# Performance work log

Hardware: AMD Instinct MI355X
Metric: run time of the kernel (lower is better)

## Reference

```python
import jax, jax.numpy as jnp
import numpy as np

EPS = 1e-12  # torch F.normalize eps


def setup_inputs() -> dict:
    key = jax.random.key(0)
    k1, k2 = jax.random.split(key)
    b, c, n, h, w = 4, 64, 25, 64, 64
    dims = 64
    x = jax.random.normal(k1, (b, c, n, h, w), dtype=jnp.float32)
    # 1x1 conv weight: Conv2d(channels, dims*3, 1, bias=False) -> [3*dims, channels]
    W = jax.random.normal(k2, (3 * dims, c), dtype=jnp.float32) * 0.05
    return {"x": x, "W": W}


def reference(x, W):
    b, c, n, h, w = x.shape
    N = n * h * w
    # 1x1 conv over channel dim (applied per (b, n) slice == plain channel matmul)
    qkv = jnp.einsum('oc,bcnhw->bonhw', W, x)  # [b, 3d, n, h, w]
    q, k, v = jnp.split(qkv, 3, axis=1)        # each [b, d, n, h, w]
    d = q.shape[1]
    q = q.reshape(b, d, N)  # b c (n h w)
    k = k.reshape(b, d, N)
    v = v.reshape(b, d, N)
    # L2-normalize each channel across the token axis (torch normalize semantics)
    qn = q / jnp.maximum(jnp.linalg.norm(q, axis=-1, keepdims=True), EPS)
    kn = k / jnp.maximum(jnp.linalg.norm(k, axis=-1, keepdims=True), EPS)
    # channel-wise cross-covariance attention: [b, d, d]
    att = jnp.einsum('bdN,beN->bde', qn, kn)
    att = jax.nn.softmax(att, axis=-1)
    out = jnp.einsum('bde,beN->bdN', att, v)   # [b, d, N]
    return out.reshape(b, d, n, h, w)
```

## Files before the change

kernel.cpp:

```cpp
#include <hip/hip_runtime.h>
#include <hip/hip_bf16.h>


#define BATCH 4
#define CH 64
#define NTOK 102400
#define DIM 64

#define GBLK 320
#define TILES_PER_BLK 5

static const size_t OFF_PART = 0;
static const size_t OFF_G    = (size_t)BATCH * GBLK * 4096;
static const size_t OFF_T1   = OFF_G  + (size_t)BATCH * 4096;
static const size_t OFF_INV  = OFF_T1 + (size_t)BATCH * 4096;
static const size_t OFF_MT   = OFF_INV + (size_t)BATCH * 128;
static const size_t WS_FLOATS_FULL = OFF_MT + (size_t)BATCH * 4096;

static const size_t SOFF_G   = 0;
static const size_t SOFF_T1  = (size_t)BATCH * 4096;
static const size_t SOFF_INV = SOFF_T1 + (size_t)BATCH * 4096;
static const size_t SOFF_MT  = SOFF_INV + (size_t)BATCH * 128;

__global__ void k_zero(float* __restrict__ p, int n) {
  int i = blockIdx.x * blockDim.x + threadIdx.x;
  if (i < n) p[i] = 0.f;
}

__device__ __forceinline__ void stage_tile64(const float* __restrict__ xrow0,
                                             float* tile, int w, int lane) {
#pragma unroll
  for (int k = 0; k < 4; ++k) {
    const int chunk = w * 4 + k;
    const int r = chunk * 4 + (lane >> 4);
    const int gp = lane & 15;
    const int gs = gp ^ ((r >> 2) & 7);
    const float* g = xrow0 + (size_t)r * NTOK + 4 * gs;
    float* l = tile + chunk * 256;
    __builtin_amdgcn_global_load_lds((const __attribute__((address_space(1))) void*)g,
                                     (__attribute__((address_space(3))) void*)l,
                                     16, 0, 0);
  }
}

__device__ __forceinline__ float4 rd_tile(const float* tile, int r, int g) {
  return *(const float4*)(tile + r * 64 + 4 * (g ^ ((r >> 2) & 7)));
}

#define VM_WAIT0() do { \
    asm volatile("s_waitcnt vmcnt(0)" ::: "memory"); \
    __builtin_amdgcn_sched_barrier(0); \
    __builtin_amdgcn_s_barrier(); \
  } while (0)

template <bool ATOMIC>
__global__ __launch_bounds__(256, 5) void k_gram(const float* __restrict__ x,
                                                 float* __restrict__ dstG) {
  __shared__ float tiles[2][4096];
  const int b = blockIdx.y;
  const int blk = blockIdx.x;
  const int tid = threadIdx.x;
  const int w = tid >> 6;
  const int lane = tid & 63;
  const int qi = w >> 1, qj = w & 1;
  const int a = lane >> 3, bb = lane & 7;

  const float* xb = x + (size_t)b * CH * NTOK;
  const int t0 = blk * (TILES_PER_BLK * 64);

  float acc[4][4] = {};

  stage_tile64(xb + t0, tiles[0], w, lane);
  VM_WAIT0();

#pragma unroll 1
  for (int i = 0; i < TILES_PER_BLK; ++i) {
    if (i + 1 < TILES_PER_BLK)
      stage_tile64(xb + t0 + 64 * (i + 1), tiles[(i + 1) & 1], w, lane);
    const float* tb = tiles[i & 1];
#pragma unroll
    for (int gt = 0; gt < 16; ++gt) {
      float4 Av[4], Bv[4];
#pragma unroll
      for (int u = 0; u < 4; ++u) Av[u] = rd_tile(tb, 32 * qi + 4 * a + u, gt);
#pragma unroll
      for (int v = 0; v < 4; ++v) Bv[v] = rd_tile(tb, 32 * qj + 4 * bb + v, gt);
#pragma unroll
      for (int u = 0; u < 4; ++u)
#pragma unroll
        for (int v = 0; v < 4; ++v) {
          float s = acc[u][v];
          s = fmaf(Av[u].x, Bv[v].x, s);
          s = fmaf(Av[u].y, Bv[v].y, s);
          s = fmaf(Av[u].z, Bv[v].z, s);
          s = fmaf(Av[u].w, Bv[v].w, s);
          acc[u][v] = s;
        }
    }
    VM_WAIT0();
  }

  if (ATOMIC) {
    float* g = dstG + (size_t)b * 4096;
#pragma unroll
    for (int u = 0; u < 4; ++u)
#pragma unroll
      for (int v = 0; v < 4; ++v)
        atomicAdd(g + (32 * qi + 4 * a + u) * 64 + 32 * qj + 4 * bb + v, acc[u][v]);
  } else {
    float* dst = dstG + ((size_t)(b * GBLK + blk)) * 4096;
#pragma unroll
    for (int u = 0; u < 4; ++u) {
      *(float4*)(dst + (32 * qi + 4 * a + u) * 64 + 32 * qj + 4 * bb) =
          make_float4(acc[u][0], acc[u][1], acc[u][2], acc[u][3]);
    }
  }
}

__global__ void k_reduceG(const float* __restrict__ partG, float* __restrict__ G) {
  const int el = blockIdx.x * 256 + threadIdx.x;
  const int b = el >> 12;
  const int e = el & 4095;
  const float* p = partG + (size_t)b * GBLK * 4096 + e;
  float s = 0.f;
#pragma unroll 8
  for (int q = 0; q < GBLK; ++q) s += p[(size_t)q * 4096];
  G[el] = s;
}

__global__ void k_rows(const float* __restrict__ W, const float* __restrict__ G,
                       float* __restrict__ T1, float* __restrict__ inv) {
  const int r = blockIdx.x;
  const int b = blockIdx.y;
  const int lane = threadIdx.x;
  const float* Wr = W + r * 64;
  const float* Gb = G + (size_t)b * 4096;
  float acc = 0.f;
#pragma unroll 8
  for (int c = 0; c < 64; ++c) acc = fmaf(Wr[c], Gb[c * 64 + lane], acc);
  float p = acc * Wr[lane];
#pragma unroll
  for (int m = 1; m < 64; m <<= 1) p += __shfl_xor(p, m, 64);
  const float nrm = sqrtf(fmaxf(p, 0.f));
  const float iv = 1.f / fmaxf(nrm, 1e-12f);
  if (r < 64) T1[((size_t)b * 64 + r) * 64 + lane] = acc * iv;
  if (lane == 0) inv[b * 128 + r] = iv;
}

__global__ void k_att(const float* __restrict__ W, const float* __restrict__ T1,
                      const float* __restrict__ inv, float* __restrict__ MT) {
  __shared__ float WkT[64][65];
  __shared__ float T1s[16][64];
  __shared__ float att[16][64];
  const int b = blockIdx.y;
  const int d0 = blockIdx.x * 16;
  const int tid = threadIdx.x;
  const int w = tid >> 6;
  const int lane = tid & 63;

#pragma unroll
  for (int r = 0; r < 16; ++r) {
    const int e = w + 4 * r;
    WkT[lane][e] = W[(64 + e) * 64 + lane];
  }
#pragma unroll
  for (int r = 0; r < 4; ++r) {
    const int dd = w + 4 * r;
    T1s[dd][lane] = T1[((size_t)b * 64 + d0 + dd) * 64 + lane];
  }
  __syncthreads();

  const float invk = inv[b * 128 + 64 + lane];
  float a[4];
#pragma unroll
  for (int it = 0; it < 4; ++it) {
    const int dd = 4 * w + it;
    float s = 0.f;
#pragma unroll 8
    for (int c = 0; c < 64; ++c) s = fmaf(T1s[dd][c], WkT[c][lane], s);
    a[it] = s * invk;
  }
#pragma unroll
  for (int it = 0; it < 4; ++it) {
    float m = a[it];
#pragma unroll
    for (int k = 1; k < 64; k <<= 1) m = fmaxf(m, __shfl_xor(m, k, 64));
    const float e = expf(a[it] - m);
    float s = e;
#pragma unroll
    for (int k = 1; k < 64; k <<= 1) s += __shfl_xor(s, k, 64);
    att[4 * w + it][lane] = e / s;
  }
  __syncthreads();
#pragma unroll
  for (int it = 0; it < 4; ++it) {
    const int dd = 4 * w + it;
    float m = 0.f;
#pragma unroll 8
    for (int e = 0; e < 64; ++e) m = fmaf(att[dd][e], W[(128 + e) * 64 + lane], m);
    MT[(size_t)b * 4096 + lane * 64 + (d0 + dd)] = m;
  }
}

__global__ __launch_bounds__(256, 5) void k_out(const float* __restrict__ x,
                                                const float* __restrict__ MT,
                                                float* __restrict__ out) {
  __shared__ float tiles[2][4096];
  const int b = blockIdx.y;
  const int blk = blockIdx.x;
  const int tid = threadIdx.x;
  const int w = tid >> 6;
  const int lane = tid & 63;
  const int a2 = lane >> 4, b2 = lane & 15;

  const float* xb = x + (size_t)b * CH * NTOK;
  const float* MTb = MT + (size_t)b * 4096;
  float* ob = out + (size_t)b * DIM * NTOK;
  const int t0 = blk * (TILES_PER_BLK * 64);
  const int row0 = 16 * w + 4 * a2;

  stage_tile64(xb + t0, tiles[0], w, lane);
  VM_WAIT0();

#pragma unroll 1
  for (int i = 0; i < TILES_PER_BLK; ++i) {
    if (i + 1 < TILES_PER_BLK)
      stage_tile64(xb + t0 + 64 * (i + 1), tiles[(i + 1) & 1], w, lane);
    const float* tb = tiles[i & 1];

    float acc[4][4] = {};
#pragma unroll 4
    for (int c = 0; c < 64; ++c) {
      const float4 Am = *(const float4*)(MTb + c * 64 + row0);
      const float4 Bx = rd_tile(tb, c, b2);
      const float am[4] = {Am.x, Am.y, Am.z, Am.w};
      const float bx[4] = {Bx.x, Bx.y, Bx.z, Bx.w};
#pragma unroll
      for (int u = 0; u < 4; ++u)
#pragma unroll
        for (int v = 0; v < 4; ++v) acc[u][v] = fmaf(am[u], bx[v], acc[u][v]);
    }

    const int tt = t0 + 64 * i + 4 * b2;
#pragma unroll
    for (int u = 0; u < 4; ++u) {
      *(float4*)(ob + (size_t)(row0 + u) * NTOK + tt) =
          make_float4(acc[u][0], acc[u][1], acc[u][2], acc[u][3]);
    }
    VM_WAIT0();
  }
}

extern "C" void kernel_launch(void* const* d_in, const int* in_sizes, int n_in,
                              void* d_out, int out_size, void* d_ws, size_t ws_size,
                              hipStream_t stream) {
  const float* x = (const float*)d_in[0];
  const float* W = (const float*)d_in[1];
  float* out = (float*)d_out;
  float* ws = (float*)d_ws;

  if (ws_size >= WS_FLOATS_FULL * sizeof(float)) {
    float* partG = ws + OFF_PART;
    float* G = ws + OFF_G;
    float* T1 = ws + OFF_T1;
    float* inv = ws + OFF_INV;
    float* MT = ws + OFF_MT;
    k_gram<false><<<dim3(GBLK, BATCH), 256, 0, stream>>>(x, partG);
    k_reduceG<<<dim3(64), 256, 0, stream>>>(partG, G);
    k_rows<<<dim3(128, BATCH), 64, 0, stream>>>(W, G, T1, inv);
    k_att<<<dim3(4, BATCH), 256, 0, stream>>>(W, T1, inv, MT);
    k_out<<<dim3(GBLK, BATCH), 256, 0, stream>>>(x, MT, out);
  } else {
    float* G = ws + SOFF_G;
    float* T1 = ws + SOFF_T1;
    float* inv = ws + SOFF_INV;
    float* MT = ws + SOFF_MT;
    k_zero<<<dim3(64), 256, 0, stream>>>(G, BATCH * 4096);
    k_gram<true><<<dim3(GBLK, BATCH), 256, 0, stream>>>(x, G);
    k_rows<<<dim3(128, BATCH), 64, 0, stream>>>(W, G, T1, inv);
    k_att<<<dim3(4, BATCH), 256, 0, stream>>>(W, T1, inv, MT);
    k_out<<<dim3(GBLK, BATCH), 256, 0, stream>>>(x, MT, out);
  }
}
```

Measured before the change: 335.7 us.

## Compute Gram matrix with split-bf16 MFMA and relayout output kernel tiles

The Gram kernel now splits each fp32 input into bf16 high and low parts and accumulates X·X^T with 16x16x32 bf16 MFMA instructions, keeping three cross terms and recovering the lo·hi term by transposing through shared memory. It also uses fewer, larger token blocks with register-prefetched double buffering. The output kernel drops the swizzled LDS layout for a linear one and remaps threads so each lane owns 4 output channels by 4 tokens. This is meant to cut the scalar FMA cost of the Gram stage, at the price of bf16-split precision (the lo·lo term is dropped) and lower occupancy.

Result: faster. 284.8 us (-15.1%).

```diff
diff --git a/kernel.cpp b/kernel.cpp
--- a/kernel.cpp
+++ b/kernel.cpp
@@ -7,11 +7,13 @@
 #define NTOK 102400
 #define DIM 64
 
-#define GBLK 320
+#define NBLK_G 200
+#define TOK_PER_G 512
+#define GBLK_OUT 320
 #define TILES_PER_BLK 5
 
 static const size_t OFF_PART = 0;
-static const size_t OFF_G    = (size_t)BATCH * GBLK * 4096;
+static const size_t OFF_G    = (size_t)BATCH * NBLK_G * 4096;
 static const size_t OFF_T1   = OFF_G  + (size_t)BATCH * 4096;
 static const size_t OFF_INV  = OFF_T1 + (size_t)BATCH * 4096;
 static const size_t OFF_MT   = OFF_INV + (size_t)BATCH * 128;
@@ -22,97 +24,135 @@
 static const size_t SOFF_INV = SOFF_T1 + (size_t)BATCH * 4096;
 static const size_t SOFF_MT  = SOFF_INV + (size_t)BATCH * 128;
 
+typedef __attribute__((ext_vector_type(8))) short short8v;
+typedef __attribute__((ext_vector_type(4))) float f32x4;
+
 __global__ void k_zero(float* __restrict__ p, int n) {
   int i = blockIdx.x * blockDim.x + threadIdx.x;
   if (i < n) p[i] = 0.f;
 }
 
-__device__ __forceinline__ void stage_tile64(const float* __restrict__ xrow0,
-                                             float* tile, int w, int lane) {
-#pragma unroll
-  for (int k = 0; k < 4; ++k) {
-    const int chunk = w * 4 + k;
-    const int r = chunk * 4 + (lane >> 4);
-    const int gp = lane & 15;
-    const int gs = gp ^ ((r >> 2) & 7);
-    const float* g = xrow0 + (size_t)r * NTOK + 4 * gs;
-    float* l = tile + chunk * 256;
-    __builtin_amdgcn_global_load_lds((const __attribute__((address_space(1))) void*)g,
-                                     (__attribute__((address_space(3))) void*)l,
-                                     16, 0, 0);
-  }
-}
-
-__device__ __forceinline__ float4 rd_tile(const float* tile, int r, int g) {
-  return *(const float4*)(tile + r * 64 + 4 * (g ^ ((r >> 2) & 7)));
-}
-
-#define VM_WAIT0() do { \
-    asm volatile("s_waitcnt vmcnt(0)" ::: "memory"); \
-    __builtin_amdgcn_sched_barrier(0); \
-    __builtin_amdgcn_s_barrier(); \
-  } while (0)
+__device__ __forceinline__ short f2bf(float f) {
+  unsigned u = __builtin_bit_cast(unsigned, f);
+  unsigned r = (u + 0x7fffu + ((u >> 16) & 1u)) >> 16;
+  return (short)r;
+}
+__device__ __forceinline__ float bf2f(short s) {
+  unsigned u = ((unsigned)(unsigned short)s) << 16;
+  return __builtin_bit_cast(float, u);
+}
 
 template <bool ATOMIC>
-__global__ __launch_bounds__(256, 5) void k_gram(const float* __restrict__ x,
+__global__ __launch_bounds__(256, 3) void k_gram(const float* __restrict__ x,
                                                  float* __restrict__ dstG) {
-  __shared__ float tiles[2][4096];
-  const int b = blockIdx.y;
-  const int blk = blockIdx.x;
+  __shared__ short his[2][4096];
+  __shared__ short los[2][4096];
+  __shared__ float p2t[64][65];
+  const int b = blockIdx.y, blk = blockIdx.x;
   const int tid = threadIdx.x;
-  const int w = tid >> 6;
-  const int lane = tid & 63;
-  const int qi = w >> 1, qj = w & 1;
-  const int a = lane >> 3, bb = lane & 7;
+  const int w = tid >> 6, lane = tid & 63;
+  const int col = lane & 15, kh = lane >> 4;
+  const int cs = tid >> 2, tq = tid & 3;
 
   const float* xb = x + (size_t)b * CH * NTOK;
-  const int t0 = blk * (TILES_PER_BLK * 64);
-
-  float acc[4][4] = {};
-
-  stage_tile64(xb + t0, tiles[0], w, lane);
-  VM_WAIT0();
+  const int t0 = blk * TOK_PER_G;
+
+  f32x4 a1[4], a2[4];
+#pragma unroll
+  for (int cb = 0; cb < 4; ++cb)
+#pragma unroll
+    for (int r = 0; r < 4; ++r) { a1[cb][r] = 0.f; a2[cb][r] = 0.f; }
+
+  const int sbase = cs * 64;
+  const int s0 = ((2 * tq) ^ (cs & 7)) << 3;
+  const int s1 = ((2 * tq + 1) ^ (cs & 7)) << 3;
+
+  {
+    const float* src = xb + (size_t)cs * NTOK + t0 + 16 * tq;
+    float4 v0 = *(const float4*)(src);
+    float4 v1 = *(const float4*)(src + 4);
+    float4 v2 = *(const float4*)(src + 8);
+    float4 v3 = *(const float4*)(src + 12);
+    float f[16] = {v0.x, v0.y, v0.z, v0.w, v1.x, v1.y, v1.z, v1.w,
+                   v2.x, v2.y, v2.z, v2.w, v3.x, v3.y, v3.z, v3.w};
+    short8v h01, h23, l01, l23;
+#pragma unroll
+    for (int j = 0; j < 8; ++j) {
+      short h = f2bf(f[j]);     h01[j] = h; l01[j] = f2bf(f[j] - bf2f(h));
+      short g = f2bf(f[j + 8]); h23[j] = g; l23[j] = f2bf(f[j + 8] - bf2f(g));
+    }
+    *(short8v*)&his[0][sbase + s0] = h01;
+    *(short8v*)&his[0][sbase + s1] = h23;
+    *(short8v*)&los[0][sbase + s0] = l01;
+    *(short8v*)&los[0][sbase + s1] = l23;
+  }
+  __syncthreads();
 
 #pragma unroll 1
-  for (int i = 0; i < TILES_PER_BLK; ++i) {
-    if (i + 1 < TILES_PER_BLK)
-      stage_tile64(xb + t0 + 64 * (i + 1), tiles[(i + 1) & 1], w, lane);
-    const float* tb = tiles[i & 1];
-#pragma unroll
-    for (int gt = 0; gt < 16; ++gt) {
-      float4 Av[4], Bv[4];
-#pragma unroll
-      for (int u = 0; u < 4; ++u) Av[u] = rd_tile(tb, 32 * qi + 4 * a + u, gt);
-#pragma unroll
-      for (int v = 0; v < 4; ++v) Bv[v] = rd_tile(tb, 32 * qj + 4 * bb + v, gt);
-#pragma unroll
-      for (int u = 0; u < 4; ++u)
-#pragma unroll
-        for (int v = 0; v < 4; ++v) {
-          float s = acc[u][v];
-          s = fmaf(Av[u].x, Bv[v].x, s);
-          s = fmaf(Av[u].y, Bv[v].y, s);
-          s = fmaf(Av[u].z, Bv[v].z, s);
-          s = fmaf(Av[u].w, Bv[v].w, s);
-          acc[u][v] = s;
-        }
-    }
-    VM_WAIT0();
-  }
-
-  if (ATOMIC) {
-    float* g = dstG + (size_t)b * 4096;
-#pragma unroll
-    for (int u = 0; u < 4; ++u)
-#pragma unroll
-      for (int v = 0; v < 4; ++v)
-        atomicAdd(g + (32 * qi + 4 * a + u) * 64 + 32 * qj + 4 * bb + v, acc[u][v]);
-  } else {
-    float* dst = dstG + ((size_t)(b * GBLK + blk)) * 4096;
-#pragma unroll
-    for (int u = 0; u < 4; ++u) {
-      *(float4*)(dst + (32 * qi + 4 * a + u) * 64 + 32 * qj + 4 * bb) =
-          make_float4(acc[u][0], acc[u][1], acc[u][2], acc[u][3]);
+  for (int i = 0; i < TOK_PER_G / 64; ++i) {
+    const int cur = i & 1;
+    const bool more = (i + 1) < TOK_PER_G / 64;
+    float4 n0, n1, n2, n3;
+    if (more) {
+      const float* src = xb + (size_t)cs * NTOK + t0 + (i + 1) * 64 + 16 * tq;
+      n0 = *(const float4*)(src);
+      n1 = *(const float4*)(src + 4);
+      n2 = *(const float4*)(src + 8);
+      n3 = *(const float4*)(src + 12);
+    }
+    const short* hp = his[cur];
+    const short* lp = los[cur];
+#pragma unroll
+    for (int kc = 0; kc < 2; ++kc) {
+      const int g = kc * 4 + kh;
+      const int rA = 16 * w + col;
+      const short8v A = *(const short8v*)&hp[rA * 64 + ((g ^ (rA & 7)) << 3)];
+#pragma unroll
+      for (int cb = 0; cb < 4; ++cb) {
+        const int rB = 16 * cb + col;
+        const int off = rB * 64 + ((g ^ (rB & 7)) << 3);
+        const short8v Bh = *(const short8v*)&hp[off];
+        const short8v Bl = *(const short8v*)&lp[off];
+        a1[cb] = __builtin_amdgcn_mfma_f32_16x16x32_bf16(A, Bh, a1[cb], 0, 0, 0);
+        a2[cb] = __builtin_amdgcn_mfma_f32_16x16x32_bf16(A, Bl, a2[cb], 0, 0, 0);
+      }
+    }
+    if (more) {
+      const int nxt = cur ^ 1;
+      float f[16] = {n0.x, n0.y, n0.z, n0.w, n1.x, n1.y, n1.z, n1.w,
+                     n2.x, n2.y, n2.z, n2.w, n3.x, n3.y, n3.z, n3.w};
+      short8v h01, h23, l01, l23;
+#pragma unroll
+      for (int j = 0; j < 8; ++j) {
+        short h = f2bf(f[j]);     h01[j] = h; l01[j] = f2bf(f[j] - bf2f(h));
+        short g2 = f2bf(f[j + 8]); h23[j] = g2; l23[j] = f2bf(f[j + 8] - bf2f(g2));
+      }
+      *(short8v*)&his[nxt][sbase + s0] = h01;
+      *(short8v*)&his[nxt][sbase + s1] = h23;
+      *(short8v*)&los[nxt][sbase + s0] = l01;
+      *(short8v*)&los[nxt][sbase + s1] = l23;
+    }
+    __syncthreads();
+  }
+
+#pragma unroll
+  for (int cb = 0; cb < 4; ++cb)
+#pragma unroll
+    for (int r = 0; r < 4; ++r)
+      p2t[16 * w + 4 * kh + r][16 * cb + col] = a2[cb][r];
+  __syncthreads();
+
+  float* dst = ATOMIC ? dstG + (size_t)b * 4096
+                      : dstG + ((size_t)(b * NBLK_G + blk)) * 4096;
+#pragma unroll
+  for (int cb = 0; cb < 4; ++cb) {
+#pragma unroll
+    for (int r = 0; r < 4; ++r) {
+      const int R = 16 * w + 4 * kh + r;
+      const int C = 16 * cb + col;
+      const float vsum = a1[cb][r] + a2[cb][r] + p2t[C][R];
+      if (ATOMIC) atomicAdd(&dst[R * 64 + C], vsum);
+      else        dst[R * 64 + C] = vsum;
     }
   }
 }
@@ -121,10 +161,10 @@
   const int el = blockIdx.x * 256 + threadIdx.x;
   const int b = el >> 12;
   const int e = el & 4095;
-  const float* p = partG + (size_t)b * GBLK * 4096 + e;
+  const float* p = partG + (size_t)b * NBLK_G * 4096 + e;
   float s = 0.f;
 #pragma unroll 8
-  for (int q = 0; q < GBLK; ++q) s += p[(size_t)q * 4096];
+  for (int q = 0; q < NBLK_G; ++q) s += p[(size_t)q * 4096];
   G[el] = s;
 }
 
@@ -202,37 +242,54 @@
   }
 }
 
-__global__ __launch_bounds__(256, 5) void k_out(const float* __restrict__ x,
+__device__ __forceinline__ void stage_lin(const float* __restrict__ xrow0,
+                                          float* tile, int w, int lane) {
+#pragma unroll
+  for (int k = 0; k < 4; ++k) {
+    const int chunk = w * 4 + k;
+    const int r = chunk * 4 + (lane >> 4);
+    const float* g = xrow0 + (size_t)r * NTOK + 4 * (lane & 15);
+    float* l = tile + chunk * 256;
+    __builtin_amdgcn_global_load_lds((const __attribute__((address_space(1))) void*)g,
+                                     (__attribute__((address_space(3))) void*)l,
+                                     16, 0, 0);
+  }
+}
+
+#define VM_WAIT0() do { \
+    asm volatile("s_waitcnt vmcnt(0)" ::: "memory"); \
+    __builtin_amdgcn_sched_barrier(0); \
+    __builtin_amdgcn_s_barrier(); \
+  } while (0)
+
+__global__ __launch_bounds__(256, 4) void k_out(const float* __restrict__ x,
                                                 const float* __restrict__ MT,
                                                 float* __restrict__ out) {
   __shared__ float tiles[2][4096];
-  const int b = blockIdx.y;
-  const int blk = blockIdx.x;
-  const int tid = threadIdx.x;
-  const int w = tid >> 6;
-  const int lane = tid & 63;
-  const int a2 = lane >> 4, b2 = lane & 15;
+  const int b = blockIdx.y, blk = blockIdx.x;
+  const int tid = threadIdx.x, w = tid >> 6, lane = tid & 63;
+  const int dg = lane & 15, tg = lane >> 4;
 
   const float* xb = x + (size_t)b * CH * NTOK;
   const float* MTb = MT + (size_t)b * 4096;
   float* ob = out + (size_t)b * DIM * NTOK;
   const int t0 = blk * (TILES_PER_BLK * 64);
-  const int row0 = 16 * w + 4 * a2;
-
-  stage_tile64(xb + t0, tiles[0], w, lane);
+  const int tof = 16 * w + 4 * tg;
+
+  stage_lin(xb + t0, tiles[0], w, lane);
   VM_WAIT0();
 
 #pragma unroll 1
   for (int i = 0; i < TILES_PER_BLK; ++i) {
     if (i + 1 < TILES_PER_BLK)
-      stage_tile64(xb + t0 + 64 * (i + 1), tiles[(i + 1) & 1], w, lane);
+      stage_lin(xb + t0 + 64 * (i + 1), tiles[(i + 1) & 1], w, lane);
     const float* tb = tiles[i & 1];
 
     float acc[4][4] = {};
-#pragma unroll 4
+#pragma unroll 8
     for (int c = 0; c < 64; ++c) {
-      const float4 Am = *(const float4*)(MTb + c * 64 + row0);
-      const float4 Bx = rd_tile(tb, c, b2);
+      const float4 Am = *(const float4*)(MTb + c * 64 + 4 * dg);
+      const float4 Bx = *(const float4*)&tb[c * 64 + tof];
       const float am[4] = {Am.x, Am.y, Am.z, Am.w};
       const float bx[4] = {Bx.x, Bx.y, Bx.z, Bx.w};
 #pragma unroll
@@ -241,10 +298,10 @@
         for (int v = 0; v < 4; ++v) acc[u][v] = fmaf(am[u], bx[v], acc[u][v]);
     }
 
-    const int tt = t0 + 64 * i + 4 * b2;
+    const int tt = t0 + 64 * i + tof;
 #pragma unroll
     for (int u = 0; u < 4; ++u) {
-      *(float4*)(ob + (size_t)(row0 + u) * NTOK + tt) =
+      *(float4*)(ob + (size_t)(4 * dg + u) * NTOK + tt) =
           make_float4(acc[u][0], acc[u][1], acc[u][2], acc[u][3]);
     }
     VM_WAIT0();
@@ -265,20 +322,20 @@
     float* T1 = ws + OFF_T1;
     float* inv = ws + OFF_INV;
     float* MT = ws + OFF_MT;
-    k_gram<false><<<dim3(GBLK, BATCH), 256, 0, stream>>>(x, partG);
+    k_gram<false><<<dim3(NBLK_G, BATCH), 256, 0, stream>>>(x, partG);
     k_reduceG<<<dim3(64), 256, 0, stream>>>(partG, G);
     k_rows<<<dim3(128, BATCH), 64, 0, stream>>>(W, G, T1, inv);
     k_att<<<dim3(4, BATCH), 256, 0, stream>>>(W, T1, inv, MT);
-    k_out<<<dim3(GBLK, BATCH), 256, 0, stream>>>(x, MT, out);
+    k_out<<<dim3(GBLK_OUT, BATCH), 256, 0, stream>>>(x, MT, out);
   } else {
     float* G = ws + SOFF_G;
     float* T1 = ws + SOFF_T1;
     float* inv = ws + SOFF_INV;
     float* MT = ws + SOFF_MT;
     k_zero<<<dim3(64), 256, 0, stream>>>(G, BATCH * 4096);
-    k_gram<true><<<dim3(GBLK, BATCH), 256, 0, stream>>>(x, G);
+    k_gram<true><<<dim3(NBLK_G, BATCH), 256, 0, stream>>>(x, G);
     k_rows<<<dim3(128, BATCH), 64, 0, stream>>>(W, G, T1, inv);
     k_att<<<dim3(4, BATCH), 256, 0, stream>>>(W, T1, inv, MT);
-    k_out<<<dim3(GBLK, BATCH), 256, 0, stream>>>(x, MT, out);
-  }
-}
+    k_out<<<dim3(GBLK_OUT, BATCH), 256, 0, stream>>>(x, MT, out);
+  }
+}
```
